# Optimization experiments

Hardware: AMD Instinct MI355X
Metric: run time of the kernel (lower is better)

## Reference

```python
import jax, jax.numpy as jnp
import numpy as np

B, LQ, LK, D = 64, 1024, 1024, 64
TEMPERATURE = 8.0  # sqrt(D)


def setup_inputs() -> dict:
    key = jax.random.key(0)
    k1, k2, k3, k4, k5, k6 = jax.random.split(key, 6)
    query = jax.random.normal(k1, (B, LQ, D), dtype=jnp.float32)
    key_t = jax.random.normal(k2, (B, LK, D), dtype=jnp.float32)
    value = jax.random.normal(k3, (B, LK, D), dtype=jnp.float32)
    query_mask = jax.random.uniform(k4, (B, LQ)) > 0.1
    key_mask = jax.random.uniform(k5, (B, LK)) > 0.1
    mask = jax.random.uniform(k6, (B, LQ, LK)) > 0.1
    return {"query": query, "key": key_t, "value": value,
            "query_mask": query_mask, "key_mask": key_mask, "mask": mask}


def reference(query, key, value, query_mask, key_mask, mask):
    # unnormalized score: bmm + scale + key/general masking with -inf
    attn = jnp.einsum('bqd,bkd->bqk', query, key) / TEMPERATURE
    neg_inf = jnp.array(-jnp.inf, dtype=attn.dtype)
    if key_mask is not None:
        attn = jnp.where(key_mask[:, None, :], attn, neg_inf)
    if mask is not None:
        attn = jnp.where(mask, attn, neg_inf)
    # softmax over key dim, then zero out masked queries
    attn = jax.nn.softmax(attn, axis=2)
    if query_mask is not None:
        attn = jnp.where(query_mask[:, :, None], attn, 0.0)
    attn_value = jnp.einsum('bqk,bkd->bqd', attn, value)
    return attn_value, attn
```

## Files before the change

### kernel.cpp

```cpp
#include <hip/hip_runtime.h>
#include <hip/hip_bf16.h>


#define NB   64
#define SLQ  1024
#define SLK  1024
#define DH   64
#define TQ   16
#define TK   64
#define NKT  16
#define MD   8
#define VSTR 76
#define PSTR 40
#define OSTR 68

typedef __attribute__((ext_vector_type(4))) float          f32x4;
typedef __attribute__((ext_vector_type(8))) __bf16         bf16x8;
typedef __attribute__((ext_vector_type(8))) unsigned short u16x8;
typedef __attribute__((ext_vector_type(4))) unsigned short u16x4;

static __device__ __forceinline__ unsigned short f2bf(float f) {
  return __builtin_bit_cast(unsigned short, (__bf16)f);
}
static __device__ __forceinline__ bf16x8 cvt8(f32x4 a, f32x4 b) {
  bf16x8 r;
#pragma unroll
  for (int i = 0; i < 4; ++i) { r[i] = (__bf16)a[i]; r[i + 4] = (__bf16)b[i]; }
  return r;
}
static __device__ __forceinline__ u16x4 cvt4(f32x4 v) {
  u16x4 h;
#pragma unroll
  for (int i = 0; i < 4; ++i) h[i] = f2bf(v[i]);
  return h;
}

__global__ __launch_bounds__(256, 3) void sdpa_fused(
    const float* __restrict__ Q, const float* __restrict__ K,
    const float* __restrict__ V, const int* __restrict__ QM,
    const int* __restrict__ KM, const int* __restrict__ MSK,
    float* __restrict__ OUT_AV, float* __restrict__ OUT_P) {
  const int g    = blockIdx.x;
  const int slot = g >> 3;
  const int b    = ((slot >> 6) << 3) | (g & 7);
  const int q0   = (slot & 63) * TQ;

  const int tid  = threadIdx.x;
  const int wave = tid >> 6;
  const int lane = tid & 63;
  const int col  = lane & 15;
  const int quad = lane >> 4;
  const int lrow = quad;
  const int lc4  = col * 4;

  __shared__ __align__(16) unsigned char RAW[25216];
  unsigned short* Vw = (unsigned short*)(RAW + wave * (32 * VSTR * 2));
  float*          Ow = (float*)(RAW + wave * (32 * VSTR * 2));
  unsigned short* Pw = (unsigned short*)(RAW + 19456) + wave * (16 * PSTR);
  float* partM = (float*)(RAW + 24576);
  float* partL = partM + 64;
  float* rowM  = partL + 64;
  float* rowS  = rowM + 16;

  const size_t mbase = ((size_t)b * SLQ + q0) * SLK;
  const f32x4* vb4 = (const f32x4*)(V + (size_t)b * SLK * DH);

  const float* qp = Q + ((size_t)b * SLQ + q0 + col) * DH + quad * 8;
  bf16x8 aq0, aq1;
  {
    f32x4 a = *(const f32x4*)qp        * 0.125f;
    f32x4 c = *(const f32x4*)(qp + 4)  * 0.125f;
    f32x4 d = *(const f32x4*)(qp + 32) * 0.125f;
    f32x4 e = *(const f32x4*)(qp + 36) * 0.125f;
    aq0 = cvt8(a, c);
    aq1 = cvt8(d, e);
  }

  const float* kp  = K + ((size_t)b * SLK + wave * 16 + col) * DH + quad * 8;
  const int*   kmp = KM + b * SLK + wave * 16 + col;
  const int*   mkp = MSK + mbase + (size_t)(quad * 4) * SLK + wave * 16 + col;

  f32x4 krg[2][4];
#pragma unroll
  for (int t = 0; t < 2; ++t) {
    const float* kq = kp + (size_t)t * (TK * DH);
    krg[t][0] = *(const f32x4*)kq;
    krg[t][1] = *(const f32x4*)(kq + 4);
    krg[t][2] = *(const f32x4*)(kq + 32);
    krg[t][3] = *(const f32x4*)(kq + 36);
  }
  int msq[MD][5];
#pragma unroll
  for (int t = 0; t < MD; ++t) {
    msq[t][0] = kmp[t * TK];
#pragma unroll
    for (int r = 0; r < 4; ++r) msq[t][r + 1] = mkp[(size_t)r * SLK + t * TK];
  }

  float sreg[NKT][4];
  unsigned mbits0 = 0u, mbits1 = 0u;
#pragma unroll
  for (int kt = 0; kt < NKT; ++kt) {
    bf16x8 bk0 = cvt8(krg[kt & 1][0], krg[kt & 1][1]);
    bf16x8 bk1 = cvt8(krg[kt & 1][2], krg[kt & 1][3]);
    if (kt < NKT - 2) {
      const float* kq = kp + (size_t)(kt + 2) * (TK * DH);
      krg[kt & 1][0] = *(const f32x4*)kq;
      krg[kt & 1][1] = *(const f32x4*)(kq + 4);
      krg[kt & 1][2] = *(const f32x4*)(kq + 32);
      krg[kt & 1][3] = *(const f32x4*)(kq + 36);
    }
    f32x4 acc = {0.f, 0.f, 0.f, 0.f};
    acc = __builtin_amdgcn_mfma_f32_16x16x32_bf16(aq0, bk0, acc, 0, 0, 0);
    acc = __builtin_amdgcn_mfma_f32_16x16x32_bf16(aq1, bk1, acc, 0, 0, 0);
#pragma unroll
    for (int r = 0; r < 4; ++r) sreg[kt][r] = acc[r];

    {
      const int km = msq[kt & (MD - 1)][0];
      unsigned bits = 0u;
#pragma unroll
      for (int r = 0; r < 4; ++r)
        bits |= (unsigned)(km & msq[kt & (MD - 1)][r + 1] & 1) << r;
      if (kt < 8) mbits0 |= bits << ((kt & 7) * 4);
      else        mbits1 |= bits << ((kt & 7) * 4);
    }
    if (kt < NKT - MD) {
      msq[kt & (MD - 1)][0] = kmp[(kt + MD) * TK];
#pragma unroll
      for (int r = 0; r < 4; ++r)
        msq[kt & (MD - 1)][r + 1] = mkp[(size_t)r * SLK + (kt + MD) * TK];
    }
  }

  f32x4 vreg[8];
#pragma unroll
  for (int j = 0; j < 8; ++j)
    vreg[j] = vb4[(size_t)((j >> 2) * TK + wave * 16 + (j & 3) * 4 + lrow) * 16 + col];

  float Mw[4], Cr[4];
#pragma unroll
  for (int r = 0; r < 4; ++r) {
    float m = sreg[0][r];
#pragma unroll
    for (int kt = 1; kt < NKT; ++kt) m = fmaxf(m, sreg[kt][r]);
#pragma unroll
    for (int off = 1; off < 16; off <<= 1) m = fmaxf(m, __shfl_xor(m, off, 64));
    Mw[r] = m;
    float l = 0.f;
#pragma unroll
    for (int kt = 0; kt < NKT; ++kt) {
      float e = __expf(sreg[kt][r] - m);
      const unsigned mb = (kt < 8) ? mbits0 : mbits1;
      e = ((mb >> ((kt & 7) * 4 + r)) & 1u) ? e : 0.f;
      sreg[kt][r] = e;
      l += e;
    }
#pragma unroll
    for (int off = 1; off < 16; off <<= 1) l += __shfl_xor(l, off, 64);
    if (col == 0) {
      partM[wave * 16 + quad * 4 + r] = m;
      partL[wave * 16 + quad * 4 + r] = l;
    }
  }
  __syncthreads();
  if (tid < TQ) {
    float M = -INFINITY, L = 0.f;
#pragma unroll
    for (int w = 0; w < 4; ++w) {
      float m_ = partM[w * 16 + tid], l_ = partL[w * 16 + tid];
      float mn = fmaxf(M, m_);
      L = L * __expf(M - mn) + l_ * __expf(m_ - mn);
      M = mn;
    }
    rowM[tid] = M;
    rowS[tid] = (QM[b * SLQ + q0 + tid] && L > 0.f) ? (1.f / L) : 0.f;
  }
  __syncthreads();
#pragma unroll
  for (int r = 0; r < 4; ++r)
    Cr[r] = __expf(Mw[r] - rowM[quad * 4 + r]) * rowS[quad * 4 + r];

  f32x4 acco[4] = {{0.f,0.f,0.f,0.f},{0.f,0.f,0.f,0.f},
                   {0.f,0.f,0.f,0.f},{0.f,0.f,0.f,0.f}};
#pragma unroll
  for (int st = 0; st < 8; ++st) {
    const int kt0 = st * 2, kt1 = kt0 + 1;
#pragma unroll
    for (int j = 0; j < 8; ++j)
      *(u16x4*)&Vw[(j * 4 + lrow) * VSTR + lc4] = cvt4(vreg[j]);

#pragma unroll
    for (int r = 0; r < 4; ++r) {
      Pw[(quad * 4 + r) * PSTR + col]      = f2bf(sreg[kt0][r] * Cr[r]);
      Pw[(quad * 4 + r) * PSTR + 16 + col] = f2bf(sreg[kt1][r] * Cr[r]);
    }

    if (st < 7) {
#pragma unroll
      for (int j = 0; j < 8; ++j)
        vreg[j] = vb4[(size_t)((st * 2 + 2 + (j >> 2)) * TK + wave * 16 + (j & 3) * 4 + lrow) * 16
                      + col];
    }

    bf16x8 ap = __builtin_bit_cast(bf16x8, *(const u16x8*)&Pw[col * PSTR + quad * 8]);
#pragma unroll
    for (int n0 = 0; n0 < 4; ++n0) {
      u16x8 rv;
#pragma unroll
      for (int j = 0; j < 8; ++j)
        rv[j] = Vw[(quad * 8 + j) * VSTR + n0 * 16 + col];
      acco[n0] = __builtin_amdgcn_mfma_f32_16x16x32_bf16(
          ap, __builtin_bit_cast(bf16x8, rv), acco[n0], 0, 0, 0);
    }
  }

  float* outp = OUT_P + mbase + (size_t)(quad * 4) * SLK + wave * 16 + col;
#pragma unroll
  for (int kt = 0; kt < NKT; ++kt)
#pragma unroll
    for (int r = 0; r < 4; ++r)
      outp[(size_t)r * SLK + kt * TK] = sreg[kt][r] * Cr[r];

#pragma unroll
  for (int n0 = 0; n0 < 4; ++n0)
#pragma unroll
    for (int r = 0; r < 4; ++r)
      Ow[(quad * 4 + r) * OSTR + n0 * 16 + col] = acco[n0][r];
  __syncthreads();
  {
    const int qq = tid >> 4, dd = (tid & 15) * 4;
    f32x4 s = {0.f, 0.f, 0.f, 0.f};
#pragma unroll
    for (int w = 0; w < 4; ++w) {
      const float* Os = (const float*)(RAW + w * (32 * VSTR * 2));
      s += *(const f32x4*)&Os[qq * OSTR + dd];
    }
    *(f32x4*)&OUT_AV[((size_t)b * SLQ + q0 + qq) * DH + dd] = s;
  }
}

extern "C" void kernel_launch(void* const* d_in, const int* in_sizes, int n_in,
                              void* d_out, int out_size, void* d_ws, size_t ws_size,
                              hipStream_t stream) {
  const float* q  = (const float*)d_in[0];
  const float* k  = (const float*)d_in[1];
  const float* v  = (const float*)d_in[2];
  const int*   qm = (const int*)d_in[3];
  const int*   km = (const int*)d_in[4];
  const int*   mk = (const int*)d_in[5];
  float* out_av = (float*)d_out;
  float* out_p  = out_av + (size_t)NB * SLQ * DH;
  sdpa_fused<<<dim3(NB * (SLQ / TQ)), dim3(256), 0, stream>>>(q, k, v, qm, km, mk, out_av, out_p);
}
```

Measured before the change: 610.3 us.

## Stream mask tiles into LDS ring via global_load_lds with manual vmcnt waits

```diff
diff --git a/kernel.cpp b/kernel.cpp
--- a/kernel.cpp
+++ b/kernel.cpp
@@ -9,15 +9,23 @@
 #define TQ   16
 #define TK   64
 #define NKT  16
-#define MD   8
 #define VSTR 76
 #define PSTR 40
 #define OSTR 68
+#define MRB  25216
 
 typedef __attribute__((ext_vector_type(4))) float          f32x4;
 typedef __attribute__((ext_vector_type(8))) __bf16         bf16x8;
 typedef __attribute__((ext_vector_type(8))) unsigned short u16x8;
 typedef __attribute__((ext_vector_type(4))) unsigned short u16x4;
+
+#define WAITV(N) asm volatile("s_waitcnt vmcnt(" #N ")" ::: "memory")
+
+static __device__ __forceinline__ void dma4(const int* g, int* l) {
+  __builtin_amdgcn_global_load_lds(
+      (const __attribute__((address_space(1))) void*)g,
+      (__attribute__((address_space(3))) void*)l, 4, 0, 0);
+}
 
 static __device__ __forceinline__ unsigned short f2bf(float f) {
   return __builtin_bit_cast(unsigned short, (__bf16)f);
@@ -53,7 +61,7 @@
   const int lrow = quad;
   const int lc4  = col * 4;
 
-  __shared__ __align__(16) unsigned char RAW[25216];
+  __shared__ __align__(16) unsigned char RAW[41600];
   unsigned short* Vw = (unsigned short*)(RAW + wave * (32 * VSTR * 2));
   float*          Ow = (float*)(RAW + wave * (32 * VSTR * 2));
   unsigned short* Pw = (unsigned short*)(RAW + 19456) + wave * (16 * PSTR);
@@ -61,6 +69,7 @@
   float* partL = partM + 64;
   float* rowM  = partL + 64;
   float* rowS  = rowM + 16;
+  int*   mring = (int*)(RAW + MRB + wave * 4096);
 
   const size_t mbase = ((size_t)b * SLQ + q0) * SLK;
   const f32x4* vb4 = (const f32x4*)(V + (size_t)b * SLK * DH);
@@ -76,9 +85,19 @@
     aq1 = cvt8(d, e);
   }
 
-  const float* kp  = K + ((size_t)b * SLK + wave * 16 + col) * DH + quad * 8;
-  const int*   kmp = KM + b * SLK + wave * 16 + col;
-  const int*   mkp = MSK + mbase + (size_t)(quad * 4) * SLK + wave * 16 + col;
+  const int* kmp = KM + b * SLK + wave * 16 + col;
+  int kmr[NKT];
+#pragma unroll
+  for (int kt = 0; kt < NKT; ++kt) kmr[kt] = kmp[kt * TK];
+
+  const int* msrc = MSK + mbase + (size_t)(lane >> 4) * SLK + wave * 16 + (lane & 15);
+#pragma unroll
+  for (int t = 0; t < 4; ++t)
+#pragma unroll
+    for (int i = 0; i < 4; ++i)
+      dma4(msrc + (size_t)i * 4 * SLK + t * TK, mring + t * 256 + i * 64);
+
+  const float* kp = K + ((size_t)b * SLK + wave * 16 + col) * DH + quad * 8;
 
   f32x4 krg[2][4];
 #pragma unroll
@@ -88,13 +107,6 @@
     krg[t][1] = *(const f32x4*)(kq + 4);
     krg[t][2] = *(const f32x4*)(kq + 32);
     krg[t][3] = *(const f32x4*)(kq + 36);
-  }
-  int msq[MD][5];
-#pragma unroll
-  for (int t = 0; t < MD; ++t) {
-    msq[t][0] = kmp[t * TK];
-#pragma unroll
-    for (int r = 0; r < 4; ++r) msq[t][r + 1] = mkp[(size_t)r * SLK + t * TK];
   }
 
   float sreg[NKT][4];
@@ -116,20 +128,30 @@
 #pragma unroll
     for (int r = 0; r < 4; ++r) sreg[kt][r] = acc[r];
 
+    if      (kt == 0)  WAITV(24);
+    else if (kt == 1)  WAITV(28);
+    else if (kt == 2)  WAITV(32);
+    else if (kt == 3)  WAITV(36);
+    else if (kt <= 12) WAITV(28);
+    else if (kt == 13) WAITV(24);
+    else if (kt == 14) WAITV(16);
+    else               WAITV(8);
+
     {
-      const int km = msq[kt & (MD - 1)][0];
+      const int* mt = mring + (kt & 3) * 256;
       unsigned bits = 0u;
 #pragma unroll
       for (int r = 0; r < 4; ++r)
-        bits |= (unsigned)(km & msq[kt & (MD - 1)][r + 1] & 1) << r;
+        bits |= (unsigned)(kmr[kt] & mt[(quad * 4 + r) * 16 + col] & 1) << r;
       if (kt < 8) mbits0 |= bits << ((kt & 7) * 4);
       else        mbits1 |= bits << ((kt & 7) * 4);
     }
-    if (kt < NKT - MD) {
-      msq[kt & (MD - 1)][0] = kmp[(kt + MD) * TK];
-#pragma unroll
-      for (int r = 0; r < 4; ++r)
-        msq[kt & (MD - 1)][r + 1] = mkp[(size_t)r * SLK + (kt + MD) * TK];
+    __builtin_amdgcn_sched_barrier(0);
+    if (kt < NKT - 4) {
+#pragma unroll
+      for (int i = 0; i < 4; ++i)
+        dma4(msrc + (size_t)i * 4 * SLK + (kt + 4) * TK,
+             mring + (kt & 3) * 256 + i * 64);
     }
   }
 
```

Measured after the change: 609.5 us. No clear change (-0.1%).

## Coalesce mask loads via ballot bitmasks, stage K and P tiles through LDS

Applied to the files above, without the earlier changes.

```diff
diff --git a/kernel.cpp b/kernel.cpp
--- a/kernel.cpp
+++ b/kernel.cpp
@@ -9,10 +9,11 @@
 #define TQ   16
 #define TK   64
 #define NKT  16
-#define MD   8
+#define KSTR 80
 #define VSTR 76
 #define PSTR 40
 #define OSTR 68
+#define PGSTR 1028
 
 typedef __attribute__((ext_vector_type(4))) float          f32x4;
 typedef __attribute__((ext_vector_type(8))) __bf16         bf16x8;
@@ -35,7 +36,7 @@
   return h;
 }
 
-__global__ __launch_bounds__(256, 3) void sdpa_fused(
+__global__ __launch_bounds__(256, 4) void sdpa_fused(
     const float* __restrict__ Q, const float* __restrict__ K,
     const float* __restrict__ V, const int* __restrict__ QM,
     const int* __restrict__ KM, const int* __restrict__ MSK,
@@ -53,16 +54,20 @@
   const int lrow = quad;
   const int lc4  = col * 4;
 
-  __shared__ __align__(16) unsigned char RAW[25216];
+  __shared__ __align__(16) unsigned char RAW[27328];
+  unsigned short* Kw = (unsigned short*)RAW + wave * (16 * KSTR);
   unsigned short* Vw = (unsigned short*)(RAW + wave * (32 * VSTR * 2));
   float*          Ow = (float*)(RAW + wave * (32 * VSTR * 2));
+  float*          Pst = (float*)RAW;
   unsigned short* Pw = (unsigned short*)(RAW + 19456) + wave * (16 * PSTR);
   float* partM = (float*)(RAW + 24576);
   float* partL = partM + 64;
   float* rowM  = partL + 64;
   float* rowS  = rowM + 16;
+  unsigned* bm = (unsigned*)(RAW + 25216);
 
   const size_t mbase = ((size_t)b * SLQ + q0) * SLK;
+  const f32x4* kb4 = (const f32x4*)(K + (size_t)b * SLK * DH);
   const f32x4* vb4 = (const f32x4*)(V + (size_t)b * SLK * DH);
 
   const float* qp = Q + ((size_t)b * SLQ + q0 + col) * DH + quad * 8;
@@ -76,67 +81,72 @@
     aq1 = cvt8(d, e);
   }
 
-  const float* kp  = K + ((size_t)b * SLK + wave * 16 + col) * DH + quad * 8;
-  const int*   kmp = KM + b * SLK + wave * 16 + col;
-  const int*   mkp = MSK + mbase + (size_t)(quad * 4) * SLK + wave * 16 + col;
-
-  f32x4 krg[2][4];
-#pragma unroll
-  for (int t = 0; t < 2; ++t) {
-    const float* kq = kp + (size_t)t * (TK * DH);
-    krg[t][0] = *(const f32x4*)kq;
-    krg[t][1] = *(const f32x4*)(kq + 4);
-    krg[t][2] = *(const f32x4*)(kq + 32);
-    krg[t][3] = *(const f32x4*)(kq + 36);
-  }
-  int msq[MD][5];
-#pragma unroll
-  for (int t = 0; t < MD; ++t) {
-    msq[t][0] = kmp[t * TK];
-#pragma unroll
-    for (int r = 0; r < 4; ++r) msq[t][r + 1] = mkp[(size_t)r * SLK + t * TK];
-  }
+  f32x4 kreg[4];
+#pragma unroll
+  for (int j = 0; j < 4; ++j)
+    kreg[j] = kb4[(size_t)(wave * 16 + j * 4 + lrow) * 16 + col];
+
+  const int* kmB = KM + b * SLK;
+  unsigned long long kmb[16];
+#pragma unroll
+  for (int c = 0; c < 16; ++c)
+    kmb[c] = __ballot(kmB[c * 64 + lane] != 0);
+
+  const int* mrow = MSK + mbase;
+#pragma unroll
+  for (int rr = 0; rr < 4; ++rr) {
+    const int row = wave * 4 + rr;
+    int mv[16];
+#pragma unroll
+    for (int c = 0; c < 16; ++c)
+      mv[c] = mrow[(size_t)row * SLK + c * 64 + lane];
+#pragma unroll
+    for (int c = 0; c < 16; ++c) {
+      unsigned long long mb_ = __ballot(mv[c] != 0) & kmb[c];
+      if (lane < 2) bm[row * 33 + c * 2 + lane] = (unsigned)(mb_ >> (lane * 32));
+    }
+  }
+  __syncthreads();
 
   float sreg[NKT][4];
-  unsigned mbits0 = 0u, mbits1 = 0u;
 #pragma unroll
   for (int kt = 0; kt < NKT; ++kt) {
-    bf16x8 bk0 = cvt8(krg[kt & 1][0], krg[kt & 1][1]);
-    bf16x8 bk1 = cvt8(krg[kt & 1][2], krg[kt & 1][3]);
-    if (kt < NKT - 2) {
-      const float* kq = kp + (size_t)(kt + 2) * (TK * DH);
-      krg[kt & 1][0] = *(const f32x4*)kq;
-      krg[kt & 1][1] = *(const f32x4*)(kq + 4);
-      krg[kt & 1][2] = *(const f32x4*)(kq + 32);
-      krg[kt & 1][3] = *(const f32x4*)(kq + 36);
-    }
+#pragma unroll
+    for (int j = 0; j < 4; ++j)
+      *(u16x4*)&Kw[(j * 4 + lrow) * KSTR + lc4] = cvt4(kreg[j]);
+
+    if (kt < NKT - 1) {
+      const int brow = (kt + 1) * TK + wave * 16;
+#pragma unroll
+      for (int j = 0; j < 4; ++j)
+        kreg[j] = kb4[(size_t)(brow + j * 4 + lrow) * 16 + col];
+    }
+
+    bf16x8 bk0 = __builtin_bit_cast(bf16x8, *(const u16x8*)&Kw[col * KSTR + quad * 8]);
+    bf16x8 bk1 = __builtin_bit_cast(bf16x8, *(const u16x8*)&Kw[col * KSTR + quad * 8 + 32]);
     f32x4 acc = {0.f, 0.f, 0.f, 0.f};
     acc = __builtin_amdgcn_mfma_f32_16x16x32_bf16(aq0, bk0, acc, 0, 0, 0);
     acc = __builtin_amdgcn_mfma_f32_16x16x32_bf16(aq1, bk1, acc, 0, 0, 0);
 #pragma unroll
     for (int r = 0; r < 4; ++r) sreg[kt][r] = acc[r];
-
-    {
-      const int km = msq[kt & (MD - 1)][0];
-      unsigned bits = 0u;
-#pragma unroll
-      for (int r = 0; r < 4; ++r)
-        bits |= (unsigned)(km & msq[kt & (MD - 1)][r + 1] & 1) << r;
-      if (kt < 8) mbits0 |= bits << ((kt & 7) * 4);
-      else        mbits1 |= bits << ((kt & 7) * 4);
-    }
-    if (kt < NKT - MD) {
-      msq[kt & (MD - 1)][0] = kmp[(kt + MD) * TK];
-#pragma unroll
-      for (int r = 0; r < 4; ++r)
-        msq[kt & (MD - 1)][r + 1] = mkp[(size_t)r * SLK + (kt + MD) * TK];
-    }
   }
 
   f32x4 vreg[8];
 #pragma unroll
   for (int j = 0; j < 8; ++j)
     vreg[j] = vb4[(size_t)((j >> 2) * TK + wave * 16 + (j & 3) * 4 + lrow) * 16 + col];
+
+  const int sh = (wave & 1) * 16 + col;
+  const int wh = wave >> 1;
+  unsigned mbits0 = 0u, mbits1 = 0u;
+#pragma unroll
+  for (int kt = 0; kt < NKT; ++kt)
+#pragma unroll
+    for (int r = 0; r < 4; ++r) {
+      unsigned bit = (bm[(quad * 4 + r) * 33 + kt * 2 + wh] >> sh) & 1u;
+      if (kt < 8) mbits0 |= bit << ((kt & 7) * 4 + r);
+      else        mbits1 |= bit << ((kt & 7) * 4 + r);
+    }
 
   float Mw[4], Cr[4];
 #pragma unroll
@@ -192,8 +202,12 @@
 
 #pragma unroll
     for (int r = 0; r < 4; ++r) {
-      Pw[(quad * 4 + r) * PSTR + col]      = f2bf(sreg[kt0][r] * Cr[r]);
-      Pw[(quad * 4 + r) * PSTR + 16 + col] = f2bf(sreg[kt1][r] * Cr[r]);
+      float p0 = sreg[kt0][r] * Cr[r];
+      float p1 = sreg[kt1][r] * Cr[r];
+      sreg[kt0][r] = p0;
+      sreg[kt1][r] = p1;
+      Pw[(quad * 4 + r) * PSTR + col]      = f2bf(p0);
+      Pw[(quad * 4 + r) * PSTR + 16 + col] = f2bf(p1);
     }
 
     if (st < 7) {
@@ -215,13 +229,6 @@
     }
   }
 
-  float* outp = OUT_P + mbase + (size_t)(quad * 4) * SLK + wave * 16 + col;
-#pragma unroll
-  for (int kt = 0; kt < NKT; ++kt)
-#pragma unroll
-    for (int r = 0; r < 4; ++r)
-      outp[(size_t)r * SLK + kt * TK] = sreg[kt][r] * Cr[r];
-
 #pragma unroll
   for (int n0 = 0; n0 < 4; ++n0)
 #pragma unroll
@@ -237,6 +244,27 @@
       s += *(const f32x4*)&Os[qq * OSTR + dd];
     }
     *(f32x4*)&OUT_AV[((size_t)b * SLQ + q0 + qq) * DH + dd] = s;
+  }
+  __syncthreads();
+
+#pragma unroll
+  for (int c = 0; c < 4; ++c) {
+    if (quad == c) {
+#pragma unroll
+      for (int kt = 0; kt < NKT; ++kt)
+#pragma unroll
+        for (int r = 0; r < 4; ++r)
+          Pst[r * PGSTR + kt * TK + wave * 16 + col] = sreg[kt][r];
+    }
+    __syncthreads();
+    {
+      float* dst = OUT_P + mbase + (size_t)(c * 4) * SLK;
+#pragma unroll
+      for (int i = 0; i < 4; ++i)
+        *(f32x4*)&dst[(size_t)i * SLK + tid * 4] =
+            *(const f32x4*)&Pst[i * PGSTR + tid * 4];
+    }
+    if (c < 3) __syncthreads();
   }
 }
 
```

Result: slower. 701.3 us (+14.9%).
